# Kernel optimization log

Hardware: AMD Instinct MI355X
Metric: run time of the kernel (lower is better)

The kernel has to match this reference:

```python
import jax, jax.numpy as jnp
import numpy as np
from jax import lax

DEPTH = 2
PATCH_SIZE = 16
PATCH_SIZE_FINAL = PATCH_SIZE // (2 ** DEPTH)  # 4
NUM_CHANNELS = 3
NUM_PATCHES = 196
NUM_PATCHES_FINAL = NUM_PATCHES * (4 ** DEPTH)  # 3136
EMB_DIM = NUM_CHANNELS * PATCH_SIZE_FINAL ** 2  # 48


def patchify(X, p):
    # X: [B, C, H, W] -> [B, (H//p)*(W//p), C, p, p], patches in row-major order
    B, C, H, W = X.shape
    eh, ew = H // p, W // p
    x = X.reshape(B, C, eh, p, ew, p)
    x = x.transpose(0, 2, 4, 1, 3, 5)  # [B, eh, ew, C, p, p]
    return x.reshape(B, eh * ew, C, p, p)


def unpatchify(x):
    # x: [B, n, C, p, p] with n = e*e -> [B, 1, C, e*p, e*p]
    B, n, C, p, _ = x.shape
    e = int(np.sqrt(n))
    img = x.reshape(B, e, e, C, p, p).transpose(0, 3, 1, 4, 2, 5).reshape(B, C, e * p, e * p)
    return img[:, None]  # [B, 1, C, H, W]


def conv_same(X, W, b):
    # NCHW conv with 3x3 kernel, 'same' padding
    y = lax.conv_general_dilated(X, W, window_strides=(1, 1), padding='SAME',
                                 dimension_numbers=('NCHW', 'OIHW', 'NCHW'))
    return y + b[None, :, None, None]


def setup_inputs() -> dict:
    key = jax.random.key(0)
    k1, k2, k3, k4 = jax.random.split(key, 4)
    return {
        'X': jax.random.normal(k1, (128, 3, 224, 224), dtype=jnp.float32),
        'conv_w': jax.random.normal(k2, (3, 3, 3, 3), dtype=jnp.float32) * 0.1,
        'conv_b': jax.random.normal(k3, (3,), dtype=jnp.float32) * 0.1,
        'pos_emb': jax.random.normal(k4, (NUM_PATCHES_FINAL, EMB_DIM), dtype=jnp.float32),
    }


def reference(X, conv_w, conv_b, pos_emb):
    B = X.shape[0]
    X = conv_same(X, conv_w, conv_b)
    # patch at fine granularity and add learned position embeddings
    pat = patchify(X, PATCH_SIZE_FINAL)                      # [B, 3136, 3, 4, 4]
    flat = pat.reshape(B, NUM_PATCHES_FINAL, EMB_DIM) + pos_emb[None]
    # unflatten + unpatch back to full image
    enc = flat.reshape(B, NUM_PATCHES_FINAL, NUM_CHANNELS, PATCH_SIZE_FINAL, PATCH_SIZE_FINAL)
    img = unpatchify(enc)                                    # [B, 1, 3, 224, 224]
    # re-patch at coarse granularity (patch() squeezes the singleton dim)
    out = patchify(img[:, 0], PATCH_SIZE)                    # [B, 196, 3, 16, 16]
    return out.reshape(B, NUM_PATCHES, NUM_CHANNELS * PATCH_SIZE ** 2)
```

## Files before the change

### kernel.cpp

```cpp
#include <hip/hip_runtime.h>

#define HW 224
#define CHW (HW*HW)
#define NBLK (28 * 128)

__global__ __launch_bounds__(256) void patch_conv_kernel(
    const float* __restrict__ X,
    const float* __restrict__ Wt,
    const float* __restrict__ Bv,
    const float* __restrict__ P,
    float* __restrict__ out)
{
    const int tid  = threadIdx.x;
    const int lane = tid & 63;
    const int wv   = tid >> 6;

    const int n    = blockIdx.x;
    const int swz  = (n & 7) * (NBLK / 8) + (n >> 3);
    const int strip = swz % 28;
    const int b     = swz / 28;

    const int y0   = strip * 8 + wv * 2;
    const int x0   = lane * 4;
    const bool act = (x0 < HW);

    float w[81];
    #pragma unroll
    for (int i = 0; i < 81; ++i) w[i] = Wt[i];

    const float* Xb = X + (size_t)b * (3 * CHW);

    float4 v[3][4];
    #pragma unroll
    for (int ci = 0; ci < 3; ++ci) {
        #pragma unroll
        for (int rj = 0; rj < 4; ++rj) {
            const int ry = y0 - 1 + rj;
            float4 t = make_float4(0.f, 0.f, 0.f, 0.f);
            if ((unsigned)ry < HW && act)
                t = *(const float4*)(Xb + ci * CHW + ry * HW + x0);
            v[ci][rj] = t;
        }
    }

    const int nf   = (y0 >> 2) * 56 + lane;
    const int sub0 = (y0 & 3) * 4;
    float4 pr[2][3];
    #pragma unroll
    for (int rr = 0; rr < 2; ++rr) {
        #pragma unroll
        for (int co = 0; co < 3; ++co) {
            float4 t = make_float4(0.f, 0.f, 0.f, 0.f);
            if (act)
                t = *(const float4*)(P + nf * 48 + co * 16 + sub0 + rr * 4);
            pr[rr][co] = t;
        }
    }

    float win[3][4][6];
    #pragma unroll
    for (int ci = 0; ci < 3; ++ci) {
        #pragma unroll
        for (int rj = 0; rj < 4; ++rj) {
            float lf = __shfl_up(v[ci][rj].w, 1);
            float rt = __shfl_down(v[ci][rj].x, 1);
            if (lane == 0) lf = 0.f;
            if (x0 + 4 >= HW) rt = 0.f;
            win[ci][rj][0] = lf;
            win[ci][rj][1] = v[ci][rj].x; win[ci][rj][2] = v[ci][rj].y;
            win[ci][rj][3] = v[ci][rj].z; win[ci][rj][4] = v[ci][rj].w;
            win[ci][rj][5] = rt;
        }
    }

    if (!act) return;

    float acc[2][3][4];
    #pragma unroll
    for (int rr = 0; rr < 2; ++rr) {
        #pragma unroll
        for (int co = 0; co < 3; ++co) {
            const float bb = Bv[co];
            acc[rr][co][0] = bb + pr[rr][co].x;
            acc[rr][co][1] = bb + pr[rr][co].y;
            acc[rr][co][2] = bb + pr[rr][co].z;
            acc[rr][co][3] = bb + pr[rr][co].w;
        }
    }

    #pragma unroll
    for (int ci = 0; ci < 3; ++ci) {
        #pragma unroll
        for (int ky = 0; ky < 3; ++ky) {
            const float* r0 = win[ci][ky];
            const float* r1 = win[ci][ky + 1];
            #pragma unroll
            for (int co = 0; co < 3; ++co) {
                const float w0 = w[((co * 3 + ci) * 3 + ky) * 3 + 0];
                const float w1 = w[((co * 3 + ci) * 3 + ky) * 3 + 1];
                const float w2 = w[((co * 3 + ci) * 3 + ky) * 3 + 2];
                #pragma unroll
                for (int j = 0; j < 4; ++j) {
                    acc[0][co][j] += w0 * r0[j] + w1 * r0[j + 1] + w2 * r0[j + 2];
                    acc[1][co][j] += w0 * r1[j] + w1 * r1[j + 1] + w2 * r1[j + 2];
                }
            }
        }
    }

    const int nc = (y0 >> 4) * 14 + (x0 >> 4);
    float* opb = out + (size_t)b * (196 * 768) + nc * 768 + (x0 & 15);
    #pragma unroll
    for (int rr = 0; rr < 2; ++rr) {
        float* op = opb + ((y0 + rr) & 15) * 16;
        #pragma unroll
        for (int co = 0; co < 3; ++co)
            *(float4*)(op + co * 256) =
                make_float4(acc[rr][co][0], acc[rr][co][1],
                            acc[rr][co][2], acc[rr][co][3]);
    }
}

extern "C" void kernel_launch(void* const* d_in, const int* in_sizes, int n_in,
                              void* d_out, int out_size, void* d_ws, size_t ws_size,
                              hipStream_t stream) {
    const float* X  = (const float*)d_in[0];
    const float* Wt = (const float*)d_in[1];
    const float* Bv = (const float*)d_in[2];
    const float* P  = (const float*)d_in[3];
    float* out = (float*)d_out;

    patch_conv_kernel<<<NBLK, 256, 0, stream>>>(X, Wt, Bv, P, out);
}
```

Measured before the change: 38.64 us.

## Stage input rows in LDS via direct global-to-LDS loads to remove redundant reads

Instead of each wave loading its own 4 input rows per channel (with 2 rows of halo overlap between waves), the block cooperatively loads the 10-row strip per channel into shared memory using global_load_lds, then each wave reads its window from LDS. This cuts redundant global/L2 traffic for the halo rows, at the cost of a block-wide barrier and LDS usage. The boundary rows are zeroed in LDS for the first and last strip.

```diff
diff --git a/kernel.cpp b/kernel.cpp
--- a/kernel.cpp
+++ b/kernel.cpp
@@ -3,6 +3,10 @@
 #define HW 224
 #define CHW (HW*HW)
 #define NBLK (28 * 128)
+#define RS 256
+
+typedef __attribute__((address_space(1))) const unsigned int guint;
+typedef __attribute__((address_space(3))) unsigned int luint;
 
 __global__ __launch_bounds__(256) void patch_conv_kernel(
     const float* __restrict__ X,
@@ -15,36 +19,54 @@
     const int lane = tid & 63;
     const int wv   = tid >> 6;
 
-    const int n    = blockIdx.x;
-    const int swz  = (n & 7) * (NBLK / 8) + (n >> 3);
+    const int n     = blockIdx.x;
+    const int swz   = (n & 7) * (NBLK / 8) + (n >> 3);
     const int strip = swz % 28;
     const int b     = swz / 28;
+    const int y0    = strip * 8;
+    const int x0    = lane * 4;
+    const bool act  = (x0 < HW);
 
-    const int y0   = strip * 8 + wv * 2;
-    const int x0   = lane * 4;
-    const bool act = (x0 < HW);
+    __shared__ float xs[3][10][RS];
+
+    if (strip == 0) {
+        for (int i = tid; i < 3 * (RS / 4); i += 256) {
+            const int ci = i >> 6, c = (i & 63) * 4;
+            *(float4*)&xs[ci][0][c] = make_float4(0.f, 0.f, 0.f, 0.f);
+        }
+    }
+    if (strip == 27) {
+        for (int i = tid; i < 3 * (RS / 4); i += 256) {
+            const int ci = i >> 6, c = (i & 63) * 4;
+            *(float4*)&xs[ci][9][c] = make_float4(0.f, 0.f, 0.f, 0.f);
+        }
+    }
+
+    const float* Xb = X + (size_t)b * (3 * CHW);
+    const int gl = (lane < 56) ? lane : 55;
+    #pragma unroll
+    for (int k = 0; k < 8; ++k) {
+        const int idx = k * 4 + wv;
+        if (idx < 30) {
+            const int ci = idx / 10, r = idx - ci * 10;
+            const int ry = y0 - 1 + r;
+            if ((unsigned)ry < HW) {
+                const float* gsrc = Xb + ci * CHW + ry * HW + gl * 4;
+                __builtin_amdgcn_global_load_lds(
+                    (guint*)(const void*)gsrc,
+                    (luint*)(void*)&xs[ci][r][0],
+                    16, 0, 0);
+            }
+        }
+    }
 
     float w[81];
     #pragma unroll
     for (int i = 0; i < 81; ++i) w[i] = Wt[i];
 
-    const float* Xb = X + (size_t)b * (3 * CHW);
-
-    float4 v[3][4];
-    #pragma unroll
-    for (int ci = 0; ci < 3; ++ci) {
-        #pragma unroll
-        for (int rj = 0; rj < 4; ++rj) {
-            const int ry = y0 - 1 + rj;
-            float4 t = make_float4(0.f, 0.f, 0.f, 0.f);
-            if ((unsigned)ry < HW && act)
-                t = *(const float4*)(Xb + ci * CHW + ry * HW + x0);
-            v[ci][rj] = t;
-        }
-    }
-
-    const int nf   = (y0 >> 2) * 56 + lane;
-    const int sub0 = (y0 & 3) * 4;
+    const int y0w  = y0 + wv * 2;
+    const int nf   = (y0w >> 2) * 56 + lane;
+    const int sub0 = (wv & 1) * 8;
     float4 pr[2][3];
     #pragma unroll
     for (int rr = 0; rr < 2; ++rr) {
@@ -57,18 +79,21 @@
         }
     }
 
+    __syncthreads();
+
     float win[3][4][6];
     #pragma unroll
     for (int ci = 0; ci < 3; ++ci) {
         #pragma unroll
         for (int rj = 0; rj < 4; ++rj) {
-            float lf = __shfl_up(v[ci][rj].w, 1);
-            float rt = __shfl_down(v[ci][rj].x, 1);
+            const float4 v = *(const float4*)&xs[ci][wv * 2 + rj][x0];
+            float lf = __shfl_up(v.w, 1);
+            float rt = __shfl_down(v.x, 1);
             if (lane == 0) lf = 0.f;
             if (x0 + 4 >= HW) rt = 0.f;
             win[ci][rj][0] = lf;
-            win[ci][rj][1] = v[ci][rj].x; win[ci][rj][2] = v[ci][rj].y;
-            win[ci][rj][3] = v[ci][rj].z; win[ci][rj][4] = v[ci][rj].w;
+            win[ci][rj][1] = v.x; win[ci][rj][2] = v.y;
+            win[ci][rj][3] = v.z; win[ci][rj][4] = v.w;
             win[ci][rj][5] = rt;
         }
     }
@@ -108,11 +133,11 @@
         }
     }
 
-    const int nc = (y0 >> 4) * 14 + (x0 >> 4);
+    const int nc = (y0w >> 4) * 14 + (x0 >> 4);
     float* opb = out + (size_t)b * (196 * 768) + nc * 768 + (x0 & 15);
     #pragma unroll
     for (int rr = 0; rr < 2; ++rr) {
-        float* op = opb + ((y0 + rr) & 15) * 16;
+        float* op = opb + ((y0w + rr) & 15) * 16;
         #pragma unroll
         for (int co = 0; co < 3; ++co)
             *(float4*)(op + co * 256) =
```

After: 46.27 us. +19.7%, slower.
